# Kernel optimization log

Measured on AMD Instinct MI355X. Metric: run time of the kernel, lower is better.

The kernel has to match this reference:

```python
import jax, jax.numpy as jnp
import numpy as np

B, L, H, E, V = 8, 8192, 512, 256, 8192  # L == V required by the pointer-gen mixing line


def setup_inputs() -> dict:
    key = jax.random.key(0)
    ks = jax.random.split(key, 20)
    f = lambda k, shape, sc=0.05: jax.random.normal(k, shape, jnp.float32) * sc
    # torch LSTM bias init: zeros, with forget-gate slice [n//4:n//2] set to 1 (applied to both b_ih and b_hh)
    lstm_bias = jnp.concatenate([jnp.zeros(H), jnp.ones(H), jnp.zeros(2 * H)]).astype(jnp.float32)
    return {
        'h': f(ks[0], (B, L, 2 * H), 1.0),
        's_h': f(ks[1], (B, H), 1.0),
        's_c': f(ks[2], (B, H), 1.0),
        'y_t_prev': jax.random.randint(ks[3], (B,), 0, V),
        'c_t_pre': f(ks[4], (B, 2 * H), 1.0),
        'coverage': jnp.zeros((B, L), jnp.float32),
        'emb': f(ks[5], (V, E)),
        'feed_W': f(ks[6], (E, E + 2 * H)),
        'feed_b': f(ks[7], (E,)),
        'Wih': f(ks[8], (4 * H, E)),
        'Whh': f(ks[9], (4 * H, H)),
        'bih': lstm_bias,
        'bhh': lstm_bias,
        'attn_W': f(ks[10], (2 * H, 4 * H + 1)),
        'attn_b': f(ks[11], (2 * H,)),
        'attn_v': f(ks[12], (2 * H,)),
        'pgen_W': f(ks[13], (4 * H + E,)),
        'pgen_b': f(ks[14], (1,)),
        'V_W': f(ks[15], (H, 3 * H)),
        'V_b': f(ks[16], (H,)),
        'Vp_W': f(ks[17], (V, H)),
        'Vp_b': f(ks[18], (V,)),
    }


def reference(h, s_h, s_c, y_t_prev, c_t_pre, coverage, emb, feed_W, feed_b,
              Wih, Whh, bih, bhh, attn_W, attn_b, attn_v, pgen_W, pgen_b,
              V_W, V_b, Vp_W, Vp_b):
    # --- input feeding ---
    x = emb[y_t_prev]                                             # (B, E)
    x = jnp.concatenate([x, c_t_pre], axis=-1) @ feed_W.T + feed_b  # (B, E)
    # --- single LSTM step (torch gate order: i, f, g, o) ---
    gates = x @ Wih.T + bih + s_h @ Whh.T + bhh                    # (B, 4H)
    i, fg, g, o = jnp.split(gates, 4, axis=-1)
    c_new = jax.nn.sigmoid(fg) * s_c + jax.nn.sigmoid(i) * jnp.tanh(g)
    h_new = jax.nn.sigmoid(o) * jnp.tanh(c_new)                    # s_t_tilde (B, H)
    s_hat = jnp.concatenate([h_new, c_new], axis=-1)               # (B, 2H)
    # --- additive attention with coverage (concat->linear split into 3 terms) ---
    Wh = attn_W[:, :2 * H]          # applied to encoder states h
    Ws = attn_W[:, 2 * H:4 * H]     # applied to decoder state s_hat
    wc = attn_W[:, 4 * H]           # applied to coverage scalar, (2H,)
    feat = jnp.tanh(jnp.einsum('bln,mn->blm', h, Wh)
                    + (s_hat @ Ws.T)[:, None, :]
                    + coverage[..., None] * wc
                    + attn_b)                                      # (B, L, 2H)
    scores = feat @ attn_v                                         # (B, L)
    attn = jax.nn.softmax(scores, axis=-1)
    c_t = jnp.einsum('bl,bln->bn', attn, h)                        # (B, 2H)
    coverage_next = coverage + attn
    # --- pointer-generator gate ---
    p_gen = jax.nn.sigmoid(jnp.concatenate([c_t, s_hat, x], axis=-1) @ pgen_W + pgen_b)[:, None]  # (B, 1)
    p_gen = p_gen[:, 0, :] if p_gen.ndim == 3 else p_gen
    # --- vocab distribution ---
    logits = (jnp.concatenate([h_new, c_t], axis=-1) @ V_W.T + V_b) @ Vp_W.T + Vp_b  # (B, V)
    P_vocab = jax.nn.softmax(logits, axis=-1)
    P_w = p_gen * P_vocab + (1.0 - p_gen) * attn                   # requires L == V
    return P_w, attn, c_t, coverage_next, h_new, c_new, p_gen
```

## Files before the change

kernel.cpp:

```cpp
#include <hip/hip_runtime.h>
#include <hip/hip_bf16.h>
#include <math.h>


#define MTOT 65536

typedef __attribute__((ext_vector_type(8))) short bf16x8;
typedef __attribute__((ext_vector_type(4))) float f32x4;

__device__ __forceinline__ float sigf(float x) { return 1.0f / (1.0f + expf(-x)); }
__device__ __forceinline__ float wave_sum(float v) {
    v += __shfl_xor(v, 1);  v += __shfl_xor(v, 2);  v += __shfl_xor(v, 4);
    v += __shfl_xor(v, 8);  v += __shfl_xor(v, 16); v += __shfl_xor(v, 32);
    return v;
}
__device__ __forceinline__ unsigned short f2bu(float f) {
    union { float f; unsigned int i; } c; c.f = f;
    unsigned int x = c.i;
    return (unsigned short)((x + 0x7fffu + ((x >> 16) & 1u)) >> 16);
}

__global__ void extract_kernel(const float* __restrict__ attn_W,
                               const float* __restrict__ attn_v,
                               unsigned short* __restrict__ Whx,
                               float* __restrict__ wcf, float* __restrict__ avf) {
    int idx0 = blockIdx.x * 1024 + threadIdx.x * 4;
    #pragma unroll
    for (int t = 0; t < 4; ++t) {
        int idx = idx0 + t;
        int m = idx >> 10, n = idx & 1023;
        Whx[idx] = f2bu(attn_W[(size_t)m * 2049 + n]);
    }
    if (blockIdx.x == 0) {
        for (int i = threadIdx.x; i < 1024; i += 256) {
            wcf[i] = attn_W[(size_t)i * 2049 + 2048];
            avf[i] = attn_v[i];
        }
    }
}

__global__ void feed_kernel(const int* __restrict__ y_prev, const float* __restrict__ emb,
                            const float* __restrict__ c_t_pre,
                            const float* __restrict__ feed_W,
                            const float* __restrict__ feed_b, float* __restrict__ xo) {
    __shared__ float cat[8 * 1280];
    int tid = threadIdx.x;
    for (int idx = tid; idx < 8 * 1280; idx += 256) {
        int b = idx / 1280, k = idx - b * 1280;
        cat[idx] = (k < 256) ? emb[(size_t)y_prev[b] * 256 + k]
                             : c_t_pre[b * 1024 + (k - 256)];
    }
    __syncthreads();
    int e = blockIdx.x * 4 + (tid >> 6);
    int lane = tid & 63;
    float acc[8] = {};
    for (int k = lane; k < 1280; k += 64) {
        float w = feed_W[(size_t)e * 1280 + k];
        #pragma unroll
        for (int b = 0; b < 8; ++b) acc[b] += w * cat[b * 1280 + k];
    }
    #pragma unroll
    for (int b = 0; b < 8; ++b) acc[b] = wave_sum(acc[b]);
    if (lane == 0) {
        float fb = feed_b[e];
        #pragma unroll
        for (int b = 0; b < 8; ++b) xo[b * 256 + e] = acc[b] + fb;
    }
}

__global__ void gates_kernel(const float* __restrict__ x, const float* __restrict__ s_h,
                             const float* __restrict__ Wih, const float* __restrict__ Whh,
                             const float* __restrict__ bih, const float* __restrict__ bhh,
                             float* __restrict__ gates) {
    __shared__ float xs[8 * 256];
    __shared__ float hs[8 * 512];
    int tid = threadIdx.x;
    for (int i = tid; i < 2048; i += 256) xs[i] = x[i];
    for (int i = tid; i < 4096; i += 256) hs[i] = s_h[i];
    __syncthreads();
    int j = blockIdx.x * 4 + (tid >> 6);
    int lane = tid & 63;
    float acc[8] = {};
    for (int k = lane; k < 256; k += 64) {
        float w = Wih[(size_t)j * 256 + k];
        #pragma unroll
        for (int b = 0; b < 8; ++b) acc[b] += w * xs[b * 256 + k];
    }
    for (int k = lane; k < 512; k += 64) {
        float w = Whh[(size_t)j * 512 + k];
        #pragma unroll
        for (int b = 0; b < 8; ++b) acc[b] += w * hs[b * 512 + k];
    }
    #pragma unroll
    for (int b = 0; b < 8; ++b) acc[b] = wave_sum(acc[b]);
    if (lane == 0) {
        float bb = bih[j] + bhh[j];
        #pragma unroll
        for (int b = 0; b < 8; ++b) gates[b * 2048 + j] = acc[b] + bb;
    }
}

__global__ void lstm_kernel(const float* __restrict__ gates, const float* __restrict__ s_c,
                            float* __restrict__ out_h, float* __restrict__ out_c,
                            float* __restrict__ shat) {
    int idx = blockIdx.x * 256 + threadIdx.x;
    int b = idx >> 9, u = idx & 511;
    const float* g = gates + b * 2048;
    float ig = sigf(g[u]), fg = sigf(g[512 + u]), gg = tanhf(g[1024 + u]), og = sigf(g[1536 + u]);
    float c = fg * s_c[idx] + ig * gg;
    float h = og * tanhf(c);
    out_h[idx] = h;
    out_c[idx] = c;
    shat[b * 1024 + u] = h;
    shat[b * 1024 + 512 + u] = c;
}

__global__ void sterm_kernel(const float* __restrict__ shat, const float* __restrict__ attn_W,
                             const float* __restrict__ attn_b, float* __restrict__ sterm) {
    __shared__ float ss[8 * 1024];
    int tid = threadIdx.x;
    for (int i = tid; i < 8192; i += 256) ss[i] = shat[i];
    __syncthreads();
    int m = blockIdx.x * 4 + (tid >> 6);
    int lane = tid & 63;
    float acc[8] = {};
    for (int k = lane; k < 1024; k += 64) {
        float w = attn_W[(size_t)m * 2049 + 1024 + k];
        #pragma unroll
        for (int b = 0; b < 8; ++b) acc[b] += w * ss[b * 1024 + k];
    }
    #pragma unroll
    for (int b = 0; b < 8; ++b) acc[b] = wave_sum(acc[b]);
    if (lane == 0) {
        float ab = attn_b[m];
        #pragma unroll
        for (int b = 0; b < 8; ++b) sterm[b * 1024 + m] = acc[b] + ab;
    }
}

__global__ __launch_bounds__(512, 4)
void attn_gemm_kernel(const float* __restrict__ h, const unsigned short* __restrict__ Whx,
                      const float* __restrict__ sterm, const float* __restrict__ coverage,
                      const float* __restrict__ wcf, const float* __restrict__ avf,
                      float* __restrict__ scores_part) {
    __shared__ uint4 As4[1024];
    __shared__ uint4 Bs4[2048];
    __shared__ float red[512];
    char* As = (char*)As4;
    char* Bs = (char*)Bs4;
    int tid = threadIdx.x;
    int id = blockIdx.x;
    int ct = (id >> 3) & 3;
    int rt = (id & 7) + ((id >> 5) << 3);
    int r0 = rt * 128, m0 = ct * 256;
    int lane = tid & 63, wid = tid >> 6;
    int wr = wid >> 2, wc = wid & 3;
    f32x4 acc[4][4] = {};

    for (int k0 = 0; k0 < 1024; k0 += 64) {
        #pragma unroll
        for (int i = 0; i < 2; ++i) {
            int cidx = i * 512 + tid;
            int row = cidx >> 3, c = cidx & 7;
            int sw = (c ^ (row & 7)) << 4;
            const float* ap = h + (size_t)(r0 + row) * 1024 + k0 + c * 8;
            uint4 a0 = *reinterpret_cast<const uint4*>(ap);
            uint4 a1 = *reinterpret_cast<const uint4*>(ap + 4);
            uint4 pk;
            pk.x = __builtin_amdgcn_perm(a0.y, a0.x, 0x07060302u);
            pk.y = __builtin_amdgcn_perm(a0.w, a0.z, 0x07060302u);
            pk.z = __builtin_amdgcn_perm(a1.y, a1.x, 0x07060302u);
            pk.w = __builtin_amdgcn_perm(a1.w, a1.z, 0x07060302u);
            *reinterpret_cast<uint4*>(As + row * 128 + sw) = pk;
        }
        #pragma unroll
        for (int i = 0; i < 4; ++i) {
            int cidx = i * 512 + tid;
            int row = cidx >> 3, c = cidx & 7;
            int sw = (c ^ (row & 7)) << 4;
            uint4 vb = *reinterpret_cast<const uint4*>(Whx + (size_t)(m0 + row) * 1024 + k0 + c * 8);
            *reinterpret_cast<uint4*>(Bs + row * 128 + sw) = vb;
        }
        __syncthreads();
        #pragma unroll
        for (int kh = 0; kh < 2; ++kh) {
            int cb = kh * 4 + (lane >> 4);
            bf16x8 af[4], bfr[4];
            #pragma unroll
            for (int mi = 0; mi < 4; ++mi) {
                int row = wr * 64 + mi * 16 + (lane & 15);
                af[mi] = *reinterpret_cast<const bf16x8*>(As + row * 128 + ((cb ^ (row & 7)) << 4));
            }
            #pragma unroll
            for (int ni = 0; ni < 4; ++ni) {
                int brow = wc * 64 + ni * 16 + (lane & 15);
                bfr[ni] = *reinterpret_cast<const bf16x8*>(Bs + brow * 128 + ((cb ^ (brow & 7)) << 4));
            }
            #pragma unroll
            for (int mi = 0; mi < 4; ++mi)
                #pragma unroll
                for (int ni = 0; ni < 4; ++ni)
                    acc[mi][ni] = __builtin_amdgcn_mfma_f32_16x16x32_bf16(af[mi], bfr[ni], acc[mi][ni], 0, 0, 0);
        }
        __syncthreads();
    }

    int b = r0 >> 13;
    float covv[4][4];
    #pragma unroll
    for (int mi = 0; mi < 4; ++mi)
        #pragma unroll
        for (int j = 0; j < 4; ++j)
            covv[mi][j] = coverage[r0 + wr * 64 + mi * 16 + ((lane >> 4) << 2) + j];
    float rs[4][4] = {};
    #pragma unroll
    for (int ni = 0; ni < 4; ++ni) {
        int m = m0 + wc * 64 + ni * 16 + (lane & 15);
        float stm = sterm[b * 1024 + m];
        float wcm = wcf[m], avm = avf[m];
        #pragma unroll
        for (int mi = 0; mi < 4; ++mi)
            #pragma unroll
            for (int j = 0; j < 4; ++j) {
                float val = acc[mi][ni][j] + stm + covv[mi][j] * wcm;
                rs[mi][j] += tanhf(val) * avm;
            }
    }
    #pragma unroll
    for (int mi = 0; mi < 4; ++mi)
        #pragma unroll
        for (int j = 0; j < 4; ++j) {
            float v = rs[mi][j];
            v += __shfl_xor(v, 1); v += __shfl_xor(v, 2);
            v += __shfl_xor(v, 4); v += __shfl_xor(v, 8);
            rs[mi][j] = v;
        }
    if ((lane & 15) == 0) {
        int g4 = lane >> 4;
        #pragma unroll
        for (int mi = 0; mi < 4; ++mi)
            #pragma unroll
            for (int j = 0; j < 4; ++j)
                red[(wr * 64 + mi * 16 + g4 * 4 + j) * 4 + wc] = rs[mi][j];
    }
    __syncthreads();
    if (tid < 128)
        scores_part[(size_t)ct * MTOT + r0 + tid] =
            red[tid * 4] + red[tid * 4 + 1] + red[tid * 4 + 2] + red[tid * 4 + 3];
}

__global__ void softmax_cov_kernel(const float* __restrict__ scores_part,
                                   const float* __restrict__ coverage,
                                   float* __restrict__ attn_out,
                                   float* __restrict__ cov_out,
                                   float* __restrict__ attnf) {
    __shared__ float s[8192];
    __shared__ float wred[4];
    int b = blockIdx.x, tid = threadIdx.x;
    int lane = tid & 63, wid = tid >> 6;
    float lmax = -1e30f;
    for (int l = tid; l < 8192; l += 256) {
        float v = 0.f;
        #pragma unroll
        for (int p = 0; p < 4; ++p) v += scores_part[(size_t)p * MTOT + b * 8192 + l];
        s[l] = v;
        lmax = fmaxf(lmax, v);
    }
    #pragma unroll
    for (int o = 32; o; o >>= 1) lmax = fmaxf(lmax, __shfl_xor(lmax, o));
    if (lane == 0) wred[wid] = lmax;
    __syncthreads();
    float bmax = fmaxf(fmaxf(wred[0], wred[1]), fmaxf(wred[2], wred[3]));
    float lsum = 0.f;
    for (int l = tid; l < 8192; l += 256) {
        float e = expf(s[l] - bmax);
        s[l] = e;
        lsum += e;
    }
    lsum = wave_sum(lsum);
    __syncthreads();
    if (lane == 0) wred[wid] = lsum;
    __syncthreads();
    float inv = 1.0f / (wred[0] + wred[1] + wred[2] + wred[3]);
    for (int l = tid; l < 8192; l += 256) {
        float a = s[l] * inv;
        attnf[b * 8192 + l] = a;
        attn_out[b * 8192 + l] = a;
        cov_out[b * 8192 + l] = coverage[b * 8192 + l] + a;
    }
}

__global__ void ct_partial_kernel(const float* __restrict__ h,
                                  const float* __restrict__ attnf, float* __restrict__ ct_part) {
    int blk = blockIdx.x;
    int b = blk >> 6, ch = blk & 63;
    int tid = threadIdx.x;
    float a0 = 0, a1 = 0, a2 = 0, a3 = 0;
    int rbase = b * 8192 + ch * 128;
    for (int l = 0; l < 128; ++l) {
        float a = attnf[rbase + l];
        float4 hv = *reinterpret_cast<const float4*>(h + (size_t)(rbase + l) * 1024 + tid * 4);
        a0 += a * hv.x; a1 += a * hv.y; a2 += a * hv.z; a3 += a * hv.w;
    }
    float4 o; o.x = a0; o.y = a1; o.z = a2; o.w = a3;
    *reinterpret_cast<float4*>(ct_part + (size_t)blk * 1024 + tid * 4) = o;
}

__global__ void ct_reduce_kernel(const float* __restrict__ ct_part, float* __restrict__ ctf,
                                 float* __restrict__ ct_out) {
    int idx = blockIdx.x * 256 + threadIdx.x;
    int b = idx >> 10, n = idx & 1023;
    const float* p = ct_part + (size_t)b * 64 * 1024 + n;
    float s = 0.f;
    #pragma unroll 8
    for (int c = 0; c < 64; ++c) s += p[c * 1024];
    ctf[idx] = s;
    ct_out[idx] = s;
}

__global__ void u_kernel(const float* __restrict__ shat, const float* __restrict__ ctf,
                         const float* __restrict__ V_W, const float* __restrict__ V_b,
                         float* __restrict__ u) {
    __shared__ float cat[8 * 1536];
    int tid = threadIdx.x;
    for (int idx = tid; idx < 8 * 1536; idx += 256) {
        int b = idx / 1536, k = idx - b * 1536;
        cat[idx] = (k < 512) ? shat[b * 1024 + k] : ctf[b * 1024 + (k - 512)];
    }
    __syncthreads();
    int i = blockIdx.x * 4 + (tid >> 6);
    int lane = tid & 63;
    float acc[8] = {};
    for (int k = lane; k < 1536; k += 64) {
        float w = V_W[(size_t)i * 1536 + k];
        #pragma unroll
        for (int b = 0; b < 8; ++b) acc[b] += w * cat[b * 1536 + k];
    }
    #pragma unroll
    for (int b = 0; b < 8; ++b) acc[b] = wave_sum(acc[b]);
    if (lane == 0) {
        float vb = V_b[i];
        #pragma unroll
        for (int b = 0; b < 8; ++b) u[b * 512 + i] = acc[b] + vb;
    }
}

__global__ void pgen_kernel(const float* __restrict__ ctf, const float* __restrict__ shat,
                            const float* __restrict__ x, const float* __restrict__ pgen_W,
                            const float* __restrict__ pgen_b,
                            float* __restrict__ pgenf, float* __restrict__ pgen_out) {
    int tid = threadIdx.x;
    int b = tid >> 6, lane = tid & 63;
    float acc = 0.f;
    for (int k = lane; k < 2304; k += 64) {
        float v;
        if (k < 1024)      v = ctf[b * 1024 + k];
        else if (k < 2048) v = shat[b * 1024 + (k - 1024)];
        else               v = x[b * 256 + (k - 2048)];
        acc += pgen_W[k] * v;
    }
    acc = wave_sum(acc);
    if (lane == 0) {
        float p = sigf(acc + pgen_b[0]);
        pgenf[b] = p;
        pgen_out[b] = p;
    }
}

__global__ void logits_kernel(const float* __restrict__ u, const float* __restrict__ Vp_W,
                              const float* __restrict__ Vp_b, float* __restrict__ logits) {
    __shared__ float us[8 * 512];
    int tid = threadIdx.x;
    for (int i = tid; i < 4096; i += 256) us[i] = u[i];
    __syncthreads();
    int v = blockIdx.x * 4 + (tid >> 6);
    int lane = tid & 63;
    float acc[8] = {};
    for (int k = lane; k < 512; k += 64) {
        float w = Vp_W[(size_t)v * 512 + k];
        #pragma unroll
        for (int b = 0; b < 8; ++b) acc[b] += w * us[b * 512 + k];
    }
    #pragma unroll
    for (int b = 0; b < 8; ++b) acc[b] = wave_sum(acc[b]);
    if (lane == 0) {
        float vb = Vp_b[v];
        #pragma unroll
        for (int b = 0; b < 8; ++b) logits[b * 8192 + v] = acc[b] + vb;
    }
}

__global__ void final_kernel(const float* __restrict__ logits, const float* __restrict__ pgenf,
                             const float* __restrict__ attnf, float* __restrict__ pw_out) {
    __shared__ float s[8192];
    __shared__ float wred[4];
    int b = blockIdx.x, tid = threadIdx.x;
    int lane = tid & 63, wid = tid >> 6;
    float lmax = -1e30f;
    for (int l = tid; l < 8192; l += 256) {
        float v = logits[b * 8192 + l];
        s[l] = v;
        lmax = fmaxf(lmax, v);
    }
    #pragma unroll
    for (int o = 32; o; o >>= 1) lmax = fmaxf(lmax, __shfl_xor(lmax, o));
    if (lane == 0) wred[wid] = lmax;
    __syncthreads();
    float bmax = fmaxf(fmaxf(wred[0], wred[1]), fmaxf(wred[2], wred[3]));
    float lsum = 0.f;
    for (int l = tid; l < 8192; l += 256) {
        float e = expf(s[l] - bmax);
        s[l] = e;
        lsum += e;
    }
    lsum = wave_sum(lsum);
    __syncthreads();
    if (lane == 0) wred[wid] = lsum;
    __syncthreads();
    float inv = 1.0f / (wred[0] + wred[1] + wred[2] + wred[3]);
    float pg = pgenf[b];
    for (int l = tid; l < 8192; l += 256) {
        float pv = s[l] * inv;
        pw_out[b * 8192 + l] = pg * pv + (1.0f - pg) * attnf[b * 8192 + l];
    }
}

extern "C" void kernel_launch(void* const* d_in, const int* in_sizes, int n_in,
                              void* d_out, int out_size, void* d_ws, size_t ws_size,
                              hipStream_t stream) {
    (void)in_sizes; (void)n_in; (void)out_size; (void)ws_size;
    const float* h        = (const float*)d_in[0];
    const float* s_h      = (const float*)d_in[1];
    const float* s_c      = (const float*)d_in[2];
    const int*   y_prev   = (const int*)d_in[3];
    const float* c_t_pre  = (const float*)d_in[4];
    const float* coverage = (const float*)d_in[5];
    const float* emb      = (const float*)d_in[6];
    const float* feed_W   = (const float*)d_in[7];
    const float* feed_b   = (const float*)d_in[8];
    const float* Wih      = (const float*)d_in[9];
    const float* Whh      = (const float*)d_in[10];
    const float* bih      = (const float*)d_in[11];
    const float* bhh      = (const float*)d_in[12];
    const float* attn_W   = (const float*)d_in[13];
    const float* attn_b   = (const float*)d_in[14];
    const float* attn_v   = (const float*)d_in[15];
    const float* pgen_W   = (const float*)d_in[16];
    const float* pgen_b   = (const float*)d_in[17];
    const float* V_W      = (const float*)d_in[18];
    const float* V_b      = (const float*)d_in[19];
    const float* Vp_W     = (const float*)d_in[20];
    const float* Vp_b     = (const float*)d_in[21];

    float* out    = (float*)d_out;
    float* o_pw   = out;
    float* o_attn = out + 65536;
    float* o_ct   = out + 131072;
    float* o_cov  = out + 139264;
    float* o_hnew = out + 204800;
    float* o_cnew = out + 208896;
    float* o_pgen = out + 212992;

    float* ws = (float*)d_ws;
    float* ws_x       = ws;
    float* ws_gates   = ws + 2048;
    float* ws_shat    = ws + 18432;
    float* ws_sterm   = ws + 26624;
    float* ws_u       = ws + 34816;
    float* ws_logits  = ws + 38912;
    float* ws_pgen    = ws + 104448;
    float* ws_wc      = ws + 105472;
    float* ws_av      = ws + 106496;
    float* ws_attnf   = ws + 107520;
    float* ws_scoresp = ws + 173056;
    float* ws_ctpart  = ws + 697344;
    float* ws_ctf     = ws + 1221632;
    unsigned short* ws_whx = (unsigned short*)(ws + 1229824);

    extract_kernel<<<1024, 256, 0, stream>>>(attn_W, attn_v, ws_whx, ws_wc, ws_av);
    feed_kernel<<<64, 256, 0, stream>>>(y_prev, emb, c_t_pre, feed_W, feed_b, ws_x);
    gates_kernel<<<512, 256, 0, stream>>>(ws_x, s_h, Wih, Whh, bih, bhh, ws_gates);
    lstm_kernel<<<16, 256, 0, stream>>>(ws_gates, s_c, o_hnew, o_cnew, ws_shat);
    sterm_kernel<<<256, 256, 0, stream>>>(ws_shat, attn_W, attn_b, ws_sterm);
    attn_gemm_kernel<<<2048, 512, 0, stream>>>(h, ws_whx, ws_sterm, coverage, ws_wc, ws_av, ws_scoresp);
    softmax_cov_kernel<<<8, 256, 0, stream>>>(ws_scoresp, coverage, o_attn, o_cov, ws_attnf);
    ct_partial_kernel<<<512, 256, 0, stream>>>(h, ws_attnf, ws_ctpart);
    ct_reduce_kernel<<<32, 256, 0, stream>>>(ws_ctpart, ws_ctf, o_ct);
    u_kernel<<<128, 256, 0, stream>>>(ws_shat, ws_ctf, V_W, V_b, ws_u);
    pgen_kernel<<<1, 512, 0, stream>>>(ws_ctf, ws_shat, ws_x, pgen_W, pgen_b, ws_pgen, o_pgen);
    logits_kernel<<<2048, 256, 0, stream>>>(ws_u, Vp_W, Vp_b, ws_logits);
    final_kernel<<<8, 256, 0, stream>>>(ws_logits, ws_pgen, ws_attnf, o_pw);
}
```

Before: 444.5 us.

## Double-buffer attention GEMM LDS tiles with register prefetch of next K-slice

Reworks the attention score GEMM main loop into a two-stage software pipeline. The next K tile of h and Whx is loaded into registers while MFMAs run on the current LDS buffer, then written to the alternate LDS buffer, so one barrier per iteration replaces two. LDS use doubles, the reduction scratch now aliases the A buffer, and launch bounds drop to one block per CU. That gives more registers for the prefetched data, at the cost of fewer resident waves to hide latency.

```diff
diff --git a/kernel.cpp b/kernel.cpp
--- a/kernel.cpp
+++ b/kernel.cpp
@@ -138,16 +138,13 @@
     }
 }
 
-__global__ __launch_bounds__(512, 4)
+__global__ __launch_bounds__(512, 1)
 void attn_gemm_kernel(const float* __restrict__ h, const unsigned short* __restrict__ Whx,
                       const float* __restrict__ sterm, const float* __restrict__ coverage,
                       const float* __restrict__ wcf, const float* __restrict__ avf,
                       float* __restrict__ scores_part) {
-    __shared__ uint4 As4[1024];
-    __shared__ uint4 Bs4[2048];
-    __shared__ float red[512];
-    char* As = (char*)As4;
-    char* Bs = (char*)Bs4;
+    __shared__ uint4 As4[2][1024];
+    __shared__ uint4 Bs4[2][2048];
     int tid = threadIdx.x;
     int id = blockIdx.x;
     int ct = (id >> 3) & 3;
@@ -157,54 +154,111 @@
     int wr = wid >> 2, wc = wid & 3;
     f32x4 acc[4][4] = {};
 
-    for (int k0 = 0; k0 < 1024; k0 += 64) {
+    int arow0 = tid >> 2,           ac0 = tid & 3;
+
+    uint4 a0[2], a1[2], bv[4];
+
+    #pragma unroll
+    for (int i = 0; i < 2; ++i) {
+        int cidx = i * 512 + tid, row = cidx >> 3, c = cidx & 7;
+        const float* ap = h + (size_t)(r0 + row) * 1024 + 0 + c * 8;
+        a0[i] = *reinterpret_cast<const uint4*>(ap);
+        a1[i] = *reinterpret_cast<const uint4*>(ap + 4);
+    }
+    #pragma unroll
+    for (int i = 0; i < 4; ++i) {
+        int cidx = i * 512 + tid, row = cidx >> 3, c = cidx & 7;
+        bv[i] = *reinterpret_cast<const uint4*>(Whx + (size_t)(m0 + row) * 1024 + 0 + c * 8);
+    }
+    {
+        char* As = (char*)As4[0];
+        char* Bs = (char*)Bs4[0];
         #pragma unroll
         for (int i = 0; i < 2; ++i) {
-            int cidx = i * 512 + tid;
-            int row = cidx >> 3, c = cidx & 7;
+            int cidx = i * 512 + tid, row = cidx >> 3, c = cidx & 7;
             int sw = (c ^ (row & 7)) << 4;
-            const float* ap = h + (size_t)(r0 + row) * 1024 + k0 + c * 8;
-            uint4 a0 = *reinterpret_cast<const uint4*>(ap);
-            uint4 a1 = *reinterpret_cast<const uint4*>(ap + 4);
             uint4 pk;
-            pk.x = __builtin_amdgcn_perm(a0.y, a0.x, 0x07060302u);
-            pk.y = __builtin_amdgcn_perm(a0.w, a0.z, 0x07060302u);
-            pk.z = __builtin_amdgcn_perm(a1.y, a1.x, 0x07060302u);
-            pk.w = __builtin_amdgcn_perm(a1.w, a1.z, 0x07060302u);
+            pk.x = __builtin_amdgcn_perm(a0[i].y, a0[i].x, 0x07060302u);
+            pk.y = __builtin_amdgcn_perm(a0[i].w, a0[i].z, 0x07060302u);
+            pk.z = __builtin_amdgcn_perm(a1[i].y, a1[i].x, 0x07060302u);
+            pk.w = __builtin_amdgcn_perm(a1[i].w, a1[i].z, 0x07060302u);
             *reinterpret_cast<uint4*>(As + row * 128 + sw) = pk;
         }
         #pragma unroll
         for (int i = 0; i < 4; ++i) {
-            int cidx = i * 512 + tid;
-            int row = cidx >> 3, c = cidx & 7;
+            int cidx = i * 512 + tid, row = cidx >> 3, c = cidx & 7;
             int sw = (c ^ (row & 7)) << 4;
-            uint4 vb = *reinterpret_cast<const uint4*>(Whx + (size_t)(m0 + row) * 1024 + k0 + c * 8);
-            *reinterpret_cast<uint4*>(Bs + row * 128 + sw) = vb;
+            *reinterpret_cast<uint4*>(Bs + row * 128 + sw) = bv[i];
+        }
+    }
+    __syncthreads();
+
+    for (int t = 0; t < 16; ++t) {
+        int buf = t & 1;
+        if (t < 15) {
+            int k0n = (t + 1) * 64;
+            #pragma unroll
+            for (int i = 0; i < 2; ++i) {
+                int cidx = i * 512 + tid, row = cidx >> 3, c = cidx & 7;
+                const float* ap = h + (size_t)(r0 + row) * 1024 + k0n + c * 8;
+                a0[i] = *reinterpret_cast<const uint4*>(ap);
+                a1[i] = *reinterpret_cast<const uint4*>(ap + 4);
+            }
+            #pragma unroll
+            for (int i = 0; i < 4; ++i) {
+                int cidx = i * 512 + tid, row = cidx >> 3, c = cidx & 7;
+                bv[i] = *reinterpret_cast<const uint4*>(Whx + (size_t)(m0 + row) * 1024 + k0n + c * 8);
+            }
+        }
+        {
+            const char* As = (const char*)As4[buf];
+            const char* Bs = (const char*)Bs4[buf];
+            #pragma unroll
+            for (int kh = 0; kh < 2; ++kh) {
+                int cb = kh * 4 + (lane >> 4);
+                bf16x8 af[4], bfr[4];
+                #pragma unroll
+                for (int mi = 0; mi < 4; ++mi) {
+                    int row = wr * 64 + mi * 16 + (lane & 15);
+                    af[mi] = *reinterpret_cast<const bf16x8*>(As + row * 128 + ((cb ^ (row & 7)) << 4));
+                }
+                #pragma unroll
+                for (int ni = 0; ni < 4; ++ni) {
+                    int brow = wc * 64 + ni * 16 + (lane & 15);
+                    bfr[ni] = *reinterpret_cast<const bf16x8*>(Bs + brow * 128 + ((cb ^ (brow & 7)) << 4));
+                }
+                #pragma unroll
+                for (int mi = 0; mi < 4; ++mi)
+                    #pragma unroll
+                    for (int ni = 0; ni < 4; ++ni)
+                        acc[mi][ni] = __builtin_amdgcn_mfma_f32_16x16x32_bf16(af[mi], bfr[ni], acc[mi][ni], 0, 0, 0);
+            }
+        }
+        if (t < 15) {
+            char* As = (char*)As4[buf ^ 1];
+            char* Bs = (char*)Bs4[buf ^ 1];
+            #pragma unroll
+            for (int i = 0; i < 2; ++i) {
+                int cidx = i * 512 + tid, row = cidx >> 3, c = cidx & 7;
+                int sw = (c ^ (row & 7)) << 4;
+                uint4 pk;
+                pk.x = __builtin_amdgcn_perm(a0[i].y, a0[i].x, 0x07060302u);
+                pk.y = __builtin_amdgcn_perm(a0[i].w, a0[i].z, 0x07060302u);
+                pk.z = __builtin_amdgcn_perm(a1[i].y, a1[i].x, 0x07060302u);
+                pk.w = __builtin_amdgcn_perm(a1[i].w, a1[i].z, 0x07060302u);
+                *reinterpret_cast<uint4*>(As + row * 128 + sw) = pk;
+            }
+            #pragma unroll
+            for (int i = 0; i < 4; ++i) {
+                int cidx = i * 512 + tid, row = cidx >> 3, c = cidx & 7;
+                int sw = (c ^ (row & 7)) << 4;
+                *reinterpret_cast<uint4*>(Bs + row * 128 + sw) = bv[i];
+            }
         }
         __syncthreads();
-        #pragma unroll
-        for (int kh = 0; kh < 2; ++kh) {
-            int cb = kh * 4 + (lane >> 4);
-            bf16x8 af[4], bfr[4];
-            #pragma unroll
-            for (int mi = 0; mi < 4; ++mi) {
-                int row = wr * 64 + mi * 16 + (lane & 15);
-                af[mi] = *reinterpret_cast<const bf16x8*>(As + row * 128 + ((cb ^ (row & 7)) << 4));
-            }
-            #pragma unroll
-            for (int ni = 0; ni < 4; ++ni) {
-                int brow = wc * 64 + ni * 16 + (lane & 15);
-                bfr[ni] = *reinterpret_cast<const bf16x8*>(Bs + brow * 128 + ((cb ^ (brow & 7)) << 4));
-            }
-            #pragma unroll
-            for (int mi = 0; mi < 4; ++mi)
-                #pragma unroll
-                for (int ni = 0; ni < 4; ++ni)
-                    acc[mi][ni] = __builtin_amdgcn_mfma_f32_16x16x32_bf16(af[mi], bfr[ni], acc[mi][ni], 0, 0, 0);
-        }
-        __syncthreads();
-    }
-
+    }
+
+    float* red = (float*)As4;
     int b = r0 >> 13;
     float covv[4][4];
     #pragma unroll
```

Result: no change. 446.7 us (+0.5%).

## Convert encoder states to bf16 once and use direct-to-LDS bf16 attention GEMM

Applied to the files above, without the earlier changes.

Adds a pass that converts h to a bf16 copy in workspace, then runs a new attention-score GEMM that streams bf16 tiles straight into swizzled LDS with global_load_lds and uses 128x128 tiles split into eight column parts. The context-vector reduction also reads the bf16 copy. The aim is to halve the bytes of h read by the GEMM and ct stages and to simplify tile loading. In exchange it adds a full read and write pass over h, needs a large workspace (with an fp32 fallback otherwise), and lowers the precision of c_t.

```diff
diff --git a/kernel.cpp b/kernel.cpp
--- a/kernel.cpp
+++ b/kernel.cpp
@@ -7,6 +7,7 @@
 
 typedef __attribute__((ext_vector_type(8))) short bf16x8;
 typedef __attribute__((ext_vector_type(4))) float f32x4;
+typedef unsigned int u32;
 
 __device__ __forceinline__ float sigf(float x) { return 1.0f / (1.0f + expf(-x)); }
 __device__ __forceinline__ float wave_sum(float v) {
@@ -19,6 +20,14 @@
     unsigned int x = c.i;
     return (unsigned short)((x + 0x7fffu + ((x >> 16) & 1u)) >> 16);
 }
+__device__ __forceinline__ float bfu(unsigned short u) {
+    union { unsigned int i; float f; } c; c.i = ((unsigned int)u) << 16; return c.f;
+}
+__device__ __forceinline__ void gl16(const void* g, void* l) {
+    __builtin_amdgcn_global_load_lds(
+        (const __attribute__((address_space(1))) u32*)g,
+        (__attribute__((address_space(3))) u32*)l, 16, 0, 0);
+}
 
 __global__ void extract_kernel(const float* __restrict__ attn_W,
                                const float* __restrict__ attn_v,
@@ -36,6 +45,21 @@
             wcf[i] = attn_W[(size_t)i * 2049 + 2048];
             avf[i] = attn_v[i];
         }
+    }
+}
+
+__global__ void h2b_kernel(const float* __restrict__ h, unsigned short* __restrict__ hb) {
+    size_t i0 = ((size_t)blockIdx.x * 256 + threadIdx.x) * 8;
+    size_t stride = (size_t)gridDim.x * 256 * 8;
+    for (size_t i = i0; i < 67108864ull; i += stride) {
+        uint4 ua = *reinterpret_cast<const uint4*>(h + i);
+        uint4 ub = *reinterpret_cast<const uint4*>(h + i + 4);
+        uint4 pk;
+        pk.x = __builtin_amdgcn_perm(ua.y, ua.x, 0x07060302u);
+        pk.y = __builtin_amdgcn_perm(ua.w, ua.z, 0x07060302u);
+        pk.z = __builtin_amdgcn_perm(ub.y, ub.x, 0x07060302u);
+        pk.w = __builtin_amdgcn_perm(ub.w, ub.z, 0x07060302u);
+        *reinterpret_cast<uint4*>(hb + i) = pk;
     }
 }
 
@@ -138,11 +162,116 @@
     }
 }
 
+__global__ __launch_bounds__(256, 3)
+void attn_gemm_bf16_kernel(const unsigned short* __restrict__ hb,
+                           const unsigned short* __restrict__ Whx,
+                           const float* __restrict__ sterm, const float* __restrict__ coverage,
+                           const float* __restrict__ wcf, const float* __restrict__ avf,
+                           float* __restrict__ scores_part) {
+    __shared__ uint4 As4[1024];
+    __shared__ uint4 Bs4[1024];
+    __shared__ float red[256];
+    char* As = (char*)As4;
+    char* Bs = (char*)Bs4;
+    int tid = threadIdx.x;
+    int id = blockIdx.x;
+    int ct = (id >> 3) & 7;
+    int rt = (id & 7) + ((id >> 6) << 3);
+    int r0 = rt * 128, m0 = ct * 128;
+    int lane = tid & 63, wid = tid >> 6;
+    int wr = wid >> 1, wc = wid & 1;
+    f32x4 acc[4][4] = {};
+
+    int lrow = lane >> 3;
+    int lsrc = (lane & 7) ^ lrow;
+
+    for (int t = 0; t < 16; ++t) {
+        int k0 = t * 64;
+        const unsigned short* hA = hb + (size_t)r0 * 1024 + k0;
+        const unsigned short* wB = Whx + (size_t)m0 * 1024 + k0;
+        #pragma unroll
+        for (int i = 0; i < 4; ++i) {
+            int row = i * 32 + wid * 8 + lrow;
+            gl16(hA + (size_t)row * 1024 + lsrc * 8, As + i * 4096 + wid * 1024);
+        }
+        #pragma unroll
+        for (int i = 0; i < 4; ++i) {
+            int row = i * 32 + wid * 8 + lrow;
+            gl16(wB + (size_t)row * 1024 + lsrc * 8, Bs + i * 4096 + wid * 1024);
+        }
+        __syncthreads();
+
+        #pragma unroll
+        for (int kh = 0; kh < 2; ++kh) {
+            int cb = kh * 4 + (lane >> 4);
+            bf16x8 af[4], bfr[4];
+            #pragma unroll
+            for (int mi = 0; mi < 4; ++mi) {
+                int row = wr * 64 + mi * 16 + (lane & 15);
+                af[mi] = *reinterpret_cast<const bf16x8*>(As + row * 128 + ((cb ^ (row & 7)) << 4));
+            }
+            #pragma unroll
+            for (int ni = 0; ni < 4; ++ni) {
+                int row = wc * 64 + ni * 16 + (lane & 15);
+                bfr[ni] = *reinterpret_cast<const bf16x8*>(Bs + row * 128 + ((cb ^ (row & 7)) << 4));
+            }
+            #pragma unroll
+            for (int mi = 0; mi < 4; ++mi)
+                #pragma unroll
+                for (int ni = 0; ni < 4; ++ni)
+                    acc[mi][ni] = __builtin_amdgcn_mfma_f32_16x16x32_bf16(af[mi], bfr[ni], acc[mi][ni], 0, 0, 0);
+        }
+        __syncthreads();
+    }
+
+    int b = r0 >> 13;
+    float covv[4][4];
+    #pragma unroll
+    for (int mi = 0; mi < 4; ++mi)
+        #pragma unroll
+        for (int j = 0; j < 4; ++j)
+            covv[mi][j] = coverage[r0 + wr * 64 + mi * 16 + ((lane >> 4) << 2) + j];
+    float rs[4][4] = {};
+    #pragma unroll
+    for (int ni = 0; ni < 4; ++ni) {
+        int m = m0 + wc * 64 + ni * 16 + (lane & 15);
+        float stm = sterm[b * 1024 + m];
+        float wcm = wcf[m], avm = avf[m];
+        #pragma unroll
+        for (int mi = 0; mi < 4; ++mi)
+            #pragma unroll
+            for (int j = 0; j < 4; ++j) {
+                float val = acc[mi][ni][j] + stm + covv[mi][j] * wcm;
+                rs[mi][j] += tanhf(val) * avm;
+            }
+    }
+    #pragma unroll
+    for (int mi = 0; mi < 4; ++mi)
+        #pragma unroll
+        for (int j = 0; j < 4; ++j) {
+            float v = rs[mi][j];
+            v += __shfl_xor(v, 1); v += __shfl_xor(v, 2);
+            v += __shfl_xor(v, 4); v += __shfl_xor(v, 8);
+            rs[mi][j] = v;
+        }
+    if ((lane & 15) == 0) {
+        int g4 = lane >> 4;
+        #pragma unroll
+        for (int mi = 0; mi < 4; ++mi)
+            #pragma unroll
+            for (int j = 0; j < 4; ++j)
+                red[(wr * 64 + mi * 16 + g4 * 4 + j) * 2 + wc] = rs[mi][j];
+    }
+    __syncthreads();
+    if (tid < 128)
+        scores_part[(size_t)ct * MTOT + r0 + tid] = red[tid * 2] + red[tid * 2 + 1];
+}
+
 __global__ __launch_bounds__(512, 4)
-void attn_gemm_kernel(const float* __restrict__ h, const unsigned short* __restrict__ Whx,
-                      const float* __restrict__ sterm, const float* __restrict__ coverage,
-                      const float* __restrict__ wcf, const float* __restrict__ avf,
-                      float* __restrict__ scores_part) {
+void attn_gemm_fb_kernel(const float* __restrict__ h, const unsigned short* __restrict__ Whx,
+                         const float* __restrict__ sterm, const float* __restrict__ coverage,
+                         const float* __restrict__ wcf, const float* __restrict__ avf,
+                         float* __restrict__ scores_part) {
     __shared__ uint4 As4[1024];
     __shared__ uint4 Bs4[2048];
     __shared__ float red[512];
@@ -253,7 +382,7 @@
                                    const float* __restrict__ coverage,
                                    float* __restrict__ attn_out,
                                    float* __restrict__ cov_out,
-                                   float* __restrict__ attnf) {
+                                   float* __restrict__ attnf, int nparts) {
     __shared__ float s[8192];
     __shared__ float wred[4];
     int b = blockIdx.x, tid = threadIdx.x;
@@ -261,8 +390,7 @@
     float lmax = -1e30f;
     for (int l = tid; l < 8192; l += 256) {
         float v = 0.f;
-        #pragma unroll
-        for (int p = 0; p < 4; ++p) v += scores_part[(size_t)p * MTOT + b * 8192 + l];
+        for (int p = 0; p < nparts; ++p) v += scores_part[(size_t)p * MTOT + b * 8192 + l];
         s[l] = v;
         lmax = fmaxf(lmax, v);
     }
@@ -288,6 +416,22 @@
         attn_out[b * 8192 + l] = a;
         cov_out[b * 8192 + l] = coverage[b * 8192 + l] + a;
     }
+}
+
+__global__ void ct_partial_bf16_kernel(const unsigned short* __restrict__ hb,
+                                       const float* __restrict__ attnf, float* __restrict__ ct_part) {
+    int blk = blockIdx.x;
+    int b = blk >> 6, ch = blk & 63;
+    int tid = threadIdx.x;
+    float a0 = 0, a1 = 0, a2 = 0, a3 = 0;
+    int rbase = b * 8192 + ch * 128;
+    for (int l = 0; l < 128; ++l) {
+        float a = attnf[rbase + l];
+        ushort4 hv = *reinterpret_cast<const ushort4*>(hb + (size_t)(rbase + l) * 1024 + tid * 4);
+        a0 += a * bfu(hv.x); a1 += a * bfu(hv.y); a2 += a * bfu(hv.z); a3 += a * bfu(hv.w);
+    }
+    float4 o; o.x = a0; o.y = a1; o.z = a2; o.w = a3;
+    *reinterpret_cast<float4*>(ct_part + (size_t)blk * 1024 + tid * 4) = o;
 }
 
 __global__ void ct_partial_kernel(const float* __restrict__ h,
@@ -428,7 +572,7 @@
 extern "C" void kernel_launch(void* const* d_in, const int* in_sizes, int n_in,
                               void* d_out, int out_size, void* d_ws, size_t ws_size,
                               hipStream_t stream) {
-    (void)in_sizes; (void)n_in; (void)out_size; (void)ws_size;
+    (void)in_sizes; (void)n_in; (void)out_size;
     const float* h        = (const float*)d_in[0];
     const float* s_h      = (const float*)d_in[1];
     const float* s_c      = (const float*)d_in[2];
@@ -476,15 +620,28 @@
     float* ws_ctpart  = ws + 697344;
     float* ws_ctf     = ws + 1221632;
     unsigned short* ws_whx = (unsigned short*)(ws + 1229824);
+    unsigned short* ws_hb  = (unsigned short*)(ws + 1754112);
+
+    const size_t NEED = (1754112ull + 33554432ull) * 4ull;
+    const bool big = ws_size >= NEED;
 
     extract_kernel<<<1024, 256, 0, stream>>>(attn_W, attn_v, ws_whx, ws_wc, ws_av);
+    if (big) h2b_kernel<<<4096, 256, 0, stream>>>(h, ws_hb);
     feed_kernel<<<64, 256, 0, stream>>>(y_prev, emb, c_t_pre, feed_W, feed_b, ws_x);
     gates_kernel<<<512, 256, 0, stream>>>(ws_x, s_h, Wih, Whh, bih, bhh, ws_gates);
     lstm_kernel<<<16, 256, 0, stream>>>(ws_gates, s_c, o_hnew, o_cnew, ws_shat);
     sterm_kernel<<<256, 256, 0, stream>>>(ws_shat, attn_W, attn_b, ws_sterm);
-    attn_gemm_kernel<<<2048, 512, 0, stream>>>(h, ws_whx, ws_sterm, coverage, ws_wc, ws_av, ws_scoresp);
-    softmax_cov_kernel<<<8, 256, 0, stream>>>(ws_scoresp, coverage, o_attn, o_cov, ws_attnf);
-    ct_partial_kernel<<<512, 256, 0, stream>>>(h, ws_attnf, ws_ctpart);
+    if (big) {
+        attn_gemm_bf16_kernel<<<4096, 256, 0, stream>>>(ws_hb, ws_whx, ws_sterm, coverage,
+                                                        ws_wc, ws_av, ws_scoresp);
+        softmax_cov_kernel<<<8, 256, 0, stream>>>(ws_scoresp, coverage, o_attn, o_cov, ws_attnf, 8);
+        ct_partial_bf16_kernel<<<512, 256, 0, stream>>>(ws_hb, ws_attnf, ws_ctpart);
+    } else {
+        attn_gemm_fb_kernel<<<2048, 512, 0, stream>>>(h, ws_whx, ws_sterm, coverage,
+                                                      ws_wc, ws_av, ws_scoresp);
+        softmax_cov_kernel<<<8, 256, 0, stream>>>(ws_scoresp, coverage, o_attn, o_cov, ws_attnf, 4);
+        ct_partial_kernel<<<512, 256, 0, stream>>>(h, ws_attnf, ws_ctpart);
+    }
     ct_reduce_kernel<<<32, 256, 0, stream>>>(ws_ctpart, ws_ctf, o_ct);
     u_kernel<<<128, 256, 0, stream>>>(ws_shat, ws_ctf, V_W, V_b, ws_u);
     pgen_kernel<<<1, 512, 0, stream>>>(ws_ctf, ws_shat, ws_x, pgen_W, pgen_b, ws_pgen, o_pgen);
```

Measured after the change: 454.0 us. +2.1%, slower.
